# Kernel optimization log

Measured on AMD Instinct MI355X. Metric: run time of the kernel, lower is better.

Reference implementation:

```python
import jax, jax.numpy as jnp
import numpy as np

HIDDEN_DIM = 2048
NUM_HEADS = 16
HEAD_DIM = HIDDEN_DIM // NUM_HEADS
BATCH = 2
SEQ = 2048


def setup_inputs() -> dict:
    key = jax.random.key(0)
    ks = jax.random.split(key, 5)
    scale = 1.0 / np.sqrt(HIDDEN_DIM)
    x = jax.random.normal(ks[0], (BATCH, SEQ, HIDDEN_DIM), dtype=jnp.float32)
    w_q = jax.random.normal(ks[1], (HIDDEN_DIM, HIDDEN_DIM), dtype=jnp.float32) * scale
    w_k = jax.random.normal(ks[2], (HIDDEN_DIM, HIDDEN_DIM), dtype=jnp.float32) * scale
    w_v = jax.random.normal(ks[3], (HIDDEN_DIM, HIDDEN_DIM), dtype=jnp.float32) * scale
    w_o = jax.random.normal(ks[4], (HIDDEN_DIM, HIDDEN_DIM), dtype=jnp.float32) * scale
    return {"x": x, "w_q": w_q, "w_k": w_k, "w_v": w_v, "w_o": w_o}


def reference(x, w_q, w_k, w_v, w_o):
    # Projections: x @ W.T  (weights stored as (out, in) like torch)
    q = jnp.einsum('bsd,ed->bse', x, w_q)
    k = jnp.einsum('bsd,ed->bse', x, w_k)
    v = jnp.einsum('bsd,ed->bse', x, w_v)
    b, s, _ = q.shape
    # split heads: (b, h, s, hd)
    q = q.reshape(b, s, NUM_HEADS, HEAD_DIM).transpose(0, 2, 1, 3)
    k = k.reshape(b, s, NUM_HEADS, HEAD_DIM).transpose(0, 2, 1, 3)
    v = v.reshape(b, s, NUM_HEADS, HEAD_DIM).transpose(0, 2, 1, 3)
    scale = 1.0 / np.sqrt(HEAD_DIM)
    # Online-softmax tiling in the source (causal=False default) is
    # mathematically identical to standard softmax attention.
    scores = jnp.einsum('bhqd,bhkd->bhqk', q, k) * scale
    p = jax.nn.softmax(scores, axis=-1)
    o = jnp.einsum('bhqk,bhkd->bhqd', p, v)
    o = o.transpose(0, 2, 1, 3).reshape(b, s, HIDDEN_DIM)
    return jnp.einsum('bsd,ed->bse', o, w_o)
```

## Files before the change

kernel.cpp:

```cpp
#include <hip/hip_runtime.h>


typedef _Float16 half8 __attribute__((ext_vector_type(8)));
typedef _Float16 half4 __attribute__((ext_vector_type(4)));
typedef float floatx4 __attribute__((ext_vector_type(4)));

__device__ __forceinline__ void async16(const void* g, void* l) {
  __builtin_amdgcn_global_load_lds((__attribute__((address_space(1))) void*)(g),
                                   (__attribute__((address_space(3))) void*)(l),
                                   16, 0, 0);
}

__global__ void cvt_all(const float* __restrict__ x, const float* __restrict__ w0,
                        const float* __restrict__ w1, const float* __restrict__ w2,
                        const float* __restrict__ w3, _Float16* __restrict__ xh,
                        _Float16* __restrict__ wh, float scale0) {
  int i = blockIdx.x * blockDim.x + threadIdx.x;
  const int XQ = 1 << 21;
  float sc = 1.0f;
  const float* src;
  _Float16* dst;
  int j;
  if (i < XQ) { src = x; dst = xh; j = i; }
  else {
    int t = i - XQ;
    int m = t >> 20;
    src = (m == 0) ? w0 : (m == 1) ? w1 : (m == 2) ? w2 : w3;
    if (m == 0) sc = scale0;
    dst = wh; j = t;
  }
  int js = (i < XQ) ? j : (j & ((1 << 20) - 1));
  float4 v = reinterpret_cast<const float4*>(src)[js];
  union { _Float16 h[4]; short4 s; } u;
  u.h[0] = (_Float16)(v.x * sc); u.h[1] = (_Float16)(v.y * sc);
  u.h[2] = (_Float16)(v.z * sc); u.h[3] = (_Float16)(v.w * sc);
  reinterpret_cast<short4*>(dst)[j] = u.s;
}

template <int MO, int NO>
__device__ __forceinline__ void mmg(floatx4 (&acc)[4][4], const half8 (&af)[2][2],
                                    const half8 (&bf)[2][2]) {
#pragma unroll
  for (int mt = 0; mt < 2; ++mt)
#pragma unroll
    for (int nt = 0; nt < 2; ++nt)
#pragma unroll
      for (int ks = 0; ks < 2; ++ks)
        acc[MO + mt][NO + nt] = __builtin_amdgcn_mfma_f32_16x16x32_f16(
            af[mt][ks], bf[nt][ks], acc[MO + mt][NO + nt], 0, 0, 0);
}

__device__ __forceinline__ void rdfrag(half8 (&f)[2][2], const _Float16* base,
                                       int r0, int r1, int ch0, int ch1) {
  f[0][0] = *reinterpret_cast<const half8*>(base + r0 * 64 + ch0);
  f[0][1] = *reinterpret_cast<const half8*>(base + r0 * 64 + ch1);
  f[1][0] = *reinterpret_cast<const half8*>(base + r1 * 64 + ch0);
  f[1][1] = *reinterpret_cast<const half8*>(base + r1 * 64 + ch1);
}

template <int OUT_MODE>
__global__ __launch_bounds__(512, 2)
void gemm_nt(const _Float16* __restrict__ A, const _Float16* __restrict__ Bw,
             void* __restrict__ Cv, void* __restrict__ Cv2) {
  __shared__ _Float16 As[2][256 * 64];
  __shared__ _Float16 Bs[2][128 * 64];
  const int tid = threadIdx.x;
  const int wave = tid >> 6, lane = tid & 63;
  const int wm = wave >> 1, wn = wave & 1;
  const int l15 = lane & 15, l4 = lane >> 4;

  const int nwg = gridDim.x << 4;
  const int orig = blockIdx.x * 16 + blockIdx.y;
  const int swz = (orig & 7) * (nwg >> 3) + (orig >> 3);
  const int bm = swz & 15, bn = swz >> 4;

  const _Float16* ag[4]; int al[4];
#pragma unroll
  for (int j = 0; j < 4; ++j) {
    int c = j * 512 + tid, row = c >> 3, g = (c & 7) ^ (row & 7);
    ag[j] = A + (size_t)(bm * 256 + row) * 2048 + g * 8;
    al[j] = c * 8;
  }
  const _Float16* bg[2]; int bl[2];
#pragma unroll
  for (int j = 0; j < 2; ++j) {
    int c = j * 512 + tid, row = c >> 3, g = (c & 7) ^ (row & 7);
    bg[j] = Bw + (size_t)(bn * 128 + row) * 2048 + g * 8;
    bl[j] = c * 8;
  }

  const int rm = wm * 16 + l15;
  const int rn = wn * 16 + l15;
  const int ch0 = (l4 ^ (l15 & 7)) * 8;
  const int ch1 = ((l4 + 4) ^ (l15 & 7)) * 8;

#pragma unroll
  for (int j = 0; j < 4; ++j) async16(ag[j], &As[0][al[j]]);
#pragma unroll
  for (int j = 0; j < 2; ++j) async16(bg[j], &Bs[0][bl[j]]);
  asm volatile("s_waitcnt vmcnt(0)" ::: "memory");
  __builtin_amdgcn_s_barrier();

  floatx4 acc[4][4] = {};
  half8 afA[2][2], afB[2][2], bfA[2][2], bfB[2][2];

#pragma unroll 2
  for (int t = 0; t < 32; ++t) {
    const _Float16* Ac = &As[t & 1][0];
    const _Float16* Bc = &Bs[t & 1][0];
    _Float16* An = &As[(t & 1) ^ 1][0];
    _Float16* Bn = &Bs[(t & 1) ^ 1][0];
    const int kn = t * 64 + 64;
    const bool st = (t < 31);

    asm volatile("s_waitcnt vmcnt(3)" ::: "memory");
    rdfrag(afA, Ac, rm, rm + 64, ch0, ch1);
    if (st) { async16(ag[0] + kn, An + al[0]); async16(ag[1] + kn, An + al[1]); }
    __builtin_amdgcn_s_barrier();
    __builtin_amdgcn_s_waitcnt(0xC07F);
    __builtin_amdgcn_s_setprio(1);
    if (t) mmg<2, 2>(acc, afB, bfB);
    __builtin_amdgcn_s_setprio(0);
    __builtin_amdgcn_s_barrier();

    asm volatile("s_waitcnt vmcnt(4)" ::: "memory");
    rdfrag(bfA, Bc, rn, rn + 32, ch0, ch1);
    if (st) async16(bg[0] + kn, Bn + bl[0]);
    __builtin_amdgcn_s_barrier();
    __builtin_amdgcn_s_waitcnt(0xC07F);
    __builtin_amdgcn_s_setprio(1);
    mmg<0, 0>(acc, afA, bfA);
    __builtin_amdgcn_s_setprio(0);
    __builtin_amdgcn_s_barrier();

    asm volatile("s_waitcnt vmcnt(3)" ::: "memory");
    rdfrag(bfB, Bc, rn + 64, rn + 96, ch0, ch1);
    if (st) async16(bg[1] + kn, Bn + bl[1]);
    __builtin_amdgcn_s_barrier();
    __builtin_amdgcn_s_waitcnt(0xC07F);
    __builtin_amdgcn_s_setprio(1);
    mmg<0, 2>(acc, afA, bfB);
    __builtin_amdgcn_s_setprio(0);
    __builtin_amdgcn_s_barrier();

    asm volatile("s_waitcnt vmcnt(2)" ::: "memory");
    rdfrag(afB, Ac, rm + 128, rm + 192, ch0, ch1);
    if (st) { async16(ag[2] + kn, An + al[2]); async16(ag[3] + kn, An + al[3]); }
    __builtin_amdgcn_s_barrier();
    __builtin_amdgcn_s_waitcnt(0xC07F);
    __builtin_amdgcn_s_setprio(1);
    mmg<2, 0>(acc, afB, bfA);
    __builtin_amdgcn_s_setprio(0);
    __builtin_amdgcn_s_barrier();
  }
  mmg<2, 2>(acc, afB, bfB);

  const int cb = bn * 128;
  if constexpr (OUT_MODE == 0) {
    if (cb < 4096) {
      _Float16* C = (_Float16*)Cv + (size_t)(cb >> 11) * (4096ull * 2048);
#pragma unroll
      for (int mt = 0; mt < 4; ++mt)
#pragma unroll
        for (int nt = 0; nt < 4; ++nt) {
          int r0 = bm * 256 + mt * 64 + wm * 16 + l4 * 4;
          int cg = (cb + nt * 32 + wn * 16 + l15) & 2047;
#pragma unroll
          for (int r = 0; r < 4; ++r)
            C[(size_t)(r0 + r) * 2048 + cg] = (_Float16)acc[mt][nt][r];
        }
    } else {
      _Float16* C = (_Float16*)Cv2;
#pragma unroll
      for (int mt = 0; mt < 4; ++mt)
#pragma unroll
        for (int nt = 0; nt < 4; ++nt) {
          int m0 = bm * 256 + mt * 64 + wm * 16 + l4 * 4;
          int d = cb + nt * 32 + wn * 16 + l15 - 4096;
          size_t base = (size_t)(m0 >> 11) * (2048ull * 2048) + (size_t)d * 2048 + (m0 & 2047);
          union { _Float16 h[4]; short4 s; } u;
#pragma unroll
          for (int r = 0; r < 4; ++r) u.h[r] = (_Float16)acc[mt][nt][r];
          *reinterpret_cast<short4*>(C + base) = u.s;
        }
    }
  } else {
    float* C = (float*)Cv;
#pragma unroll
    for (int mt = 0; mt < 4; ++mt)
#pragma unroll
      for (int nt = 0; nt < 4; ++nt) {
        int r0 = bm * 256 + mt * 64 + wm * 16 + l4 * 4;
        int cg = cb + nt * 32 + wn * 16 + l15;
#pragma unroll
        for (int r = 0; r < 4; ++r)
          C[(size_t)(r0 + r) * 2048 + cg] = acc[mt][nt][r];
      }
  }
}

__global__ __launch_bounds__(256, 2)
void flash_attn(const _Float16* __restrict__ Q, const _Float16* __restrict__ Kg,
                const _Float16* __restrict__ Vt, _Float16* __restrict__ O) {
  __shared__ _Float16 Ks[64 * 128];
  __shared__ _Float16 Vs[128 * 64];
  __shared__ _Float16 Ps[128 * 64];
  const int tid = threadIdx.x, wave = tid >> 6, lane = tid & 63;
  const int l15 = lane & 15, l4 = lane >> 4;
  const int bh = blockIdx.y, b = bh >> 4, h = bh & 15;
  const int q0 = blockIdx.x * 128;

  const _Float16* Qp = Q + ((size_t)(b * 2048 + q0 + wave * 32)) * 2048 + h * 128;
  const _Float16* Kp = Kg + (size_t)b * 2048 * 2048 + h * 128;
  const _Float16* Vp = Vt + (size_t)b * 2048 * 2048 + (size_t)(h * 128) * 2048;

  half8 qf[2][4];
#pragma unroll
  for (int qt = 0; qt < 2; ++qt)
#pragma unroll
    for (int ks = 0; ks < 4; ++ks)
      qf[qt][ks] = *reinterpret_cast<const half8*>(
          Qp + (size_t)(qt * 16 + l15) * 2048 + ks * 32 + l4 * 8);

  floatx4 oacc[2][8] = {};
  float lsumq[2] = {0.f, 0.f};

  for (int k0 = 0; k0 < 2048; k0 += 64) {
    __syncthreads();
#pragma unroll
    for (int i = 0; i < 4; ++i) {
      int c = i * 256 + tid;
      int row = c >> 4, cc = c & 15;
      int g = cc ^ (row & 15);
      async16(Kp + (size_t)(k0 + row) * 2048 + g * 8, &Ks[c * 8]);
    }
#pragma unroll
    for (int i = 0; i < 4; ++i) {
      int c = i * 256 + tid;
      int row = c >> 3, cc = c & 7;
      int g = cc ^ (row & 7);
      async16(Vp + (size_t)row * 2048 + k0 + g * 8, &Vs[c * 8]);
    }
    __syncthreads();

    floatx4 sacc[4][2] = {};
#pragma unroll
    for (int ks = 0; ks < 4; ++ks) {
      half8 kf[4];
#pragma unroll
      for (int st = 0; st < 4; ++st) {
        int row = st * 16 + l15;
        int ch = (ks * 4 + l4) ^ l15;
        kf[st] = *reinterpret_cast<const half8*>(&Ks[row * 128 + ch * 8]);
      }
#pragma unroll
      for (int st = 0; st < 4; ++st)
#pragma unroll
        for (int qt = 0; qt < 2; ++qt)
          sacc[st][qt] = __builtin_amdgcn_mfma_f32_16x16x32_f16(kf[st], qf[qt][ks], sacc[st][qt], 0, 0, 0);
    }

#pragma unroll
    for (int qt = 0; qt < 2; ++qt)
#pragma unroll
      for (int st = 0; st < 4; ++st) {
        float p0 = exp2f(sacc[st][qt][0]);
        float p1 = exp2f(sacc[st][qt][1]);
        float p2 = exp2f(sacc[st][qt][2]);
        float p3 = exp2f(sacc[st][qt][3]);
        lsumq[qt] += (p0 + p1) + (p2 + p3);
        half4 pv;
        pv[0] = (_Float16)p0; pv[1] = (_Float16)p1;
        pv[2] = (_Float16)p2; pv[3] = (_Float16)p3;
        int ch = (st * 2 + (l4 >> 1)) ^ (l15 & 7);
        *reinterpret_cast<half4*>(
            &Ps[(wave * 32 + qt * 16 + l15) * 64 + ch * 8 + (l4 & 1) * 4]) = pv;
      }

    __builtin_amdgcn_s_waitcnt(0xC07F);

#pragma unroll
    for (int ks2 = 0; ks2 < 2; ++ks2) {
      half8 pf[2];
#pragma unroll
      for (int mt = 0; mt < 2; ++mt)
        pf[mt] = *reinterpret_cast<const half8*>(
            &Ps[(wave * 32 + mt * 16 + l15) * 64 + (((ks2 * 4 + l4) ^ (l15 & 7)) * 8)]);
#pragma unroll
      for (int nt2 = 0; nt2 < 8; ++nt2) {
        int row = nt2 * 16 + l15;
        int ch = (ks2 * 4 + l4) ^ (row & 7);
        half8 vf = *reinterpret_cast<const half8*>(&Vs[row * 64 + ch * 8]);
#pragma unroll
        for (int mt = 0; mt < 2; ++mt)
          oacc[mt][nt2] = __builtin_amdgcn_mfma_f32_16x16x32_f16(pf[mt], vf, oacc[mt][nt2], 0, 0, 0);
      }
    }
  }

#pragma unroll
  for (int qt = 0; qt < 2; ++qt) {
    lsumq[qt] += __shfl_xor(lsumq[qt], 16);
    lsumq[qt] += __shfl_xor(lsumq[qt], 32);
  }

  _Float16* Op = O + ((size_t)(b * 2048 + q0 + wave * 32)) * 2048 + h * 128;
#pragma unroll
  for (int mt = 0; mt < 2; ++mt)
#pragma unroll
    for (int r = 0; r < 4; ++r) {
      float inv = 1.0f / __shfl(lsumq[mt], l4 * 4 + r);
#pragma unroll
      for (int nt2 = 0; nt2 < 8; ++nt2) {
        int row = mt * 16 + l4 * 4 + r;
        int col = nt2 * 16 + l15;
        Op[(size_t)row * 2048 + col] = (_Float16)(oacc[mt][nt2][r] * inv);
      }
    }
}

extern "C" void kernel_launch(void* const* d_in, const int* in_sizes, int n_in,
                              void* d_out, int out_size, void* d_ws, size_t ws_size,
                              hipStream_t stream) {
  const float* x = (const float*)d_in[0];
  const float* wq = (const float*)d_in[1];
  const float* wk = (const float*)d_in[2];
  const float* wv = (const float*)d_in[3];
  const float* wo = (const float*)d_in[4];
  float* out = (float*)d_out;

  const size_t XN = (size_t)4096 * 2048;
  const size_t WN = (size_t)2048 * 2048;
  _Float16* xh = (_Float16*)d_ws;
  _Float16* qh = xh + XN;
  _Float16* vth = xh + 3 * XN;
  _Float16* oh = xh + 4 * XN;
  _Float16* wqh = xh + 5 * XN;

  const float SM_SCALE = 0.08838834764831845f * 1.4426950408889634f;

  cvt_all<<<dim3(24576), 256, 0, stream>>>(x, wq, wk, wv, wo, xh, wqh, SM_SCALE);
  gemm_nt<0><<<dim3(48, 16), 512, 0, stream>>>(xh, wqh, qh, vth);
  flash_attn<<<dim3(16, 32), 256, 0, stream>>>(qh, qh + XN, vth, oh);
  gemm_nt<2><<<dim3(16, 16), 512, 0, stream>>>(oh, wqh + 3 * WN, out, nullptr);
}
```

Measured before the change: 409.1 us.

## Enlarge projection GEMM tile to 256x256 with a 2x4 wave layout

The NT GEMM block tile grows from 256x128 to 256x256. Eight waves are arranged 2x4 and each wave holds an 8x4 set of 16x16 accumulators. The K loop is restructured into four phases with explicit vmcnt waits and a peeled final iteration, and the grid becomes 1D with a compile-time N-block count. The aim is to raise arithmetic intensity and cut global and LDS traffic per FLOP. In exchange, LDS use doubles to about 128KB per block, register pressure rises under the (512,2) launch bounds with a risk of spills, and the output projection launches only 128 blocks on a 256-CU device.

```diff
diff --git a/kernel.cpp b/kernel.cpp
--- a/kernel.cpp
+++ b/kernel.cpp
@@ -37,134 +37,156 @@
   reinterpret_cast<short4*>(dst)[j] = u.s;
 }
 
+__device__ __forceinline__ void rdA4(half8 (&f)[4][2], const _Float16* base,
+                                     int ch0, int ch1) {
+#pragma unroll
+  for (int mt = 0; mt < 4; ++mt) {
+    f[mt][0] = *reinterpret_cast<const half8*>(base + mt * 2048 + ch0);
+    f[mt][1] = *reinterpret_cast<const half8*>(base + mt * 2048 + ch1);
+  }
+}
+__device__ __forceinline__ void rdB2(half8 (&f)[2][2], const _Float16* base,
+                                     int ch0, int ch1) {
+#pragma unroll
+  for (int nt = 0; nt < 2; ++nt) {
+    f[nt][0] = *reinterpret_cast<const half8*>(base + nt * 4096 + ch0);
+    f[nt][1] = *reinterpret_cast<const half8*>(base + nt * 4096 + ch1);
+  }
+}
 template <int MO, int NO>
-__device__ __forceinline__ void mmg(floatx4 (&acc)[4][4], const half8 (&af)[2][2],
-                                    const half8 (&bf)[2][2]) {
-#pragma unroll
-  for (int mt = 0; mt < 2; ++mt)
-#pragma unroll
-    for (int nt = 0; nt < 2; ++nt)
-#pragma unroll
-      for (int ks = 0; ks < 2; ++ks)
+__device__ __forceinline__ void mmg16(floatx4 (&acc)[8][4], const half8 (&af)[4][2],
+                                      const half8 (&bf)[2][2]) {
+#pragma unroll
+  for (int kk = 0; kk < 2; ++kk)
+#pragma unroll
+    for (int mt = 0; mt < 4; ++mt)
+#pragma unroll
+      for (int nt = 0; nt < 2; ++nt)
         acc[MO + mt][NO + nt] = __builtin_amdgcn_mfma_f32_16x16x32_f16(
-            af[mt][ks], bf[nt][ks], acc[MO + mt][NO + nt], 0, 0, 0);
-}
-
-__device__ __forceinline__ void rdfrag(half8 (&f)[2][2], const _Float16* base,
-                                       int r0, int r1, int ch0, int ch1) {
-  f[0][0] = *reinterpret_cast<const half8*>(base + r0 * 64 + ch0);
-  f[0][1] = *reinterpret_cast<const half8*>(base + r0 * 64 + ch1);
-  f[1][0] = *reinterpret_cast<const half8*>(base + r1 * 64 + ch0);
-  f[1][1] = *reinterpret_cast<const half8*>(base + r1 * 64 + ch1);
-}
-
-template <int OUT_MODE>
+            af[mt][kk], bf[nt][kk], acc[MO + mt][NO + nt], 0, 0, 0);
+}
+
+template <int OUT_MODE, int NBN>
 __global__ __launch_bounds__(512, 2)
 void gemm_nt(const _Float16* __restrict__ A, const _Float16* __restrict__ Bw,
              void* __restrict__ Cv, void* __restrict__ Cv2) {
   __shared__ _Float16 As[2][256 * 64];
-  __shared__ _Float16 Bs[2][128 * 64];
+  __shared__ _Float16 Bs[2][256 * 64];
   const int tid = threadIdx.x;
   const int wave = tid >> 6, lane = tid & 63;
-  const int wm = wave >> 1, wn = wave & 1;
+  const int wm = wave >> 2, wn = wave & 3;
   const int l15 = lane & 15, l4 = lane >> 4;
 
-  const int nwg = gridDim.x << 4;
-  const int orig = blockIdx.x * 16 + blockIdx.y;
+  const int nwg = NBN * 16;
+  const int orig = blockIdx.x;
   const int swz = (orig & 7) * (nwg >> 3) + (orig >> 3);
-  const int bm = swz & 15, bn = swz >> 4;
-
-  const _Float16* ag[4]; int al[4];
-#pragma unroll
-  for (int j = 0; j < 4; ++j) {
-    int c = j * 512 + tid, row = c >> 3, g = (c & 7) ^ (row & 7);
-    ag[j] = A + (size_t)(bm * 256 + row) * 2048 + g * 8;
-    al[j] = c * 8;
-  }
-  const _Float16* bg[2]; int bl[2];
-#pragma unroll
-  for (int j = 0; j < 2; ++j) {
-    int c = j * 512 + tid, row = c >> 3, g = (c & 7) ^ (row & 7);
-    bg[j] = Bw + (size_t)(bn * 128 + row) * 2048 + g * 8;
-    bl[j] = c * 8;
-  }
-
-  const int rm = wm * 16 + l15;
-  const int rn = wn * 16 + l15;
+  const int bn = swz % NBN, bm = swz / NBN;
+
+  const int srow = tid >> 3;
+  const int g = (tid & 7) ^ (srow & 7);
+  const _Float16* ags = A + (size_t)(bm * 256 + srow) * 2048 + g * 8;
+  const _Float16* bgs = Bw + (size_t)(bn * 256 + srow) * 2048 + g * 8;
+  const int ldst = tid * 8;
+
+  const int arow = wm * 16 + l15;
+  const int brow = wn * 16 + l15;
   const int ch0 = (l4 ^ (l15 & 7)) * 8;
   const int ch1 = ((l4 + 4) ^ (l15 & 7)) * 8;
 
 #pragma unroll
-  for (int j = 0; j < 4; ++j) async16(ag[j], &As[0][al[j]]);
-#pragma unroll
-  for (int j = 0; j < 2; ++j) async16(bg[j], &Bs[0][bl[j]]);
+  for (int j = 0; j < 4; ++j) {
+    async16(ags + (size_t)j * 131072, &As[0][j * 4096 + ldst]);
+    async16(bgs + (size_t)j * 131072, &Bs[0][j * 4096 + ldst]);
+  }
   asm volatile("s_waitcnt vmcnt(0)" ::: "memory");
   __builtin_amdgcn_s_barrier();
 
-  floatx4 acc[4][4] = {};
-  half8 afA[2][2], afB[2][2], bfA[2][2], bfB[2][2];
-
-#pragma unroll 2
-  for (int t = 0; t < 32; ++t) {
-    const _Float16* Ac = &As[t & 1][0];
-    const _Float16* Bc = &Bs[t & 1][0];
-    _Float16* An = &As[(t & 1) ^ 1][0];
-    _Float16* Bn = &Bs[(t & 1) ^ 1][0];
+  floatx4 acc[8][4] = {};
+  half8 afA[4][2], afB[4][2], bfA[2][2], bfB[2][2];
+
+  for (int t = 0; t < 31; ++t) {
+    const int cur = t & 1, nxt = cur ^ 1;
     const int kn = t * 64 + 64;
-    const bool st = (t < 31);
-
-    asm volatile("s_waitcnt vmcnt(3)" ::: "memory");
-    rdfrag(afA, Ac, rm, rm + 64, ch0, ch1);
-    if (st) { async16(ag[0] + kn, An + al[0]); async16(ag[1] + kn, An + al[1]); }
+    const _Float16* Ab = &As[cur][arow * 64];
+    const _Float16* Bb = &Bs[cur][brow * 64];
+    _Float16* Asn = &As[nxt][ldst];
+    _Float16* Bsn = &Bs[nxt][ldst];
+
+    rdA4(afA, Ab, ch0, ch1);
+    async16(ags + kn, Asn);
+    async16(ags + 131072 + kn, Asn + 4096);
     __builtin_amdgcn_s_barrier();
     __builtin_amdgcn_s_waitcnt(0xC07F);
     __builtin_amdgcn_s_setprio(1);
-    if (t) mmg<2, 2>(acc, afB, bfB);
+    if (t) mmg16<4, 2>(acc, afB, bfB);
     __builtin_amdgcn_s_setprio(0);
-    __builtin_amdgcn_s_barrier();
-
+    asm volatile("s_waitcnt vmcnt(6)" ::: "memory");
+    __builtin_amdgcn_s_barrier();
+
+    rdB2(bfA, Bb, ch0, ch1);
+    async16(bgs + kn, Bsn);
+    async16(bgs + 131072 + kn, Bsn + 4096);
+    __builtin_amdgcn_s_barrier();
+    __builtin_amdgcn_s_waitcnt(0xC07F);
+    __builtin_amdgcn_s_setprio(1);
+    mmg16<0, 0>(acc, afA, bfA);
+    __builtin_amdgcn_s_setprio(0);
+    asm volatile("s_waitcnt vmcnt(6)" ::: "memory");
+    __builtin_amdgcn_s_barrier();
+
+    rdB2(bfB, Bb + 8192, ch0, ch1);
+    async16(bgs + 262144 + kn, Bsn + 8192);
+    async16(bgs + 393216 + kn, Bsn + 12288);
+    __builtin_amdgcn_s_barrier();
+    __builtin_amdgcn_s_waitcnt(0xC07F);
+    __builtin_amdgcn_s_setprio(1);
+    mmg16<0, 2>(acc, afA, bfB);
+    __builtin_amdgcn_s_setprio(0);
+    asm volatile("s_waitcnt vmcnt(6)" ::: "memory");
+    __builtin_amdgcn_s_barrier();
+
+    rdA4(afB, Ab + 8192, ch0, ch1);
+    async16(ags + 262144 + kn, Asn + 8192);
+    async16(ags + 393216 + kn, Asn + 12288);
+    __builtin_amdgcn_s_barrier();
+    __builtin_amdgcn_s_waitcnt(0xC07F);
+    __builtin_amdgcn_s_setprio(1);
+    mmg16<4, 0>(acc, afB, bfA);
+    __builtin_amdgcn_s_setprio(0);
+    asm volatile("s_waitcnt vmcnt(6)" ::: "memory");
+    __builtin_amdgcn_s_barrier();
+  }
+
+  {
+    const _Float16* Ab = &As[1][arow * 64];
+    const _Float16* Bb = &Bs[1][brow * 64];
+    rdA4(afA, Ab, ch0, ch1);
+    mmg16<4, 2>(acc, afB, bfB);
     asm volatile("s_waitcnt vmcnt(4)" ::: "memory");
-    rdfrag(bfA, Bc, rn, rn + 32, ch0, ch1);
-    if (st) async16(bg[0] + kn, Bn + bl[0]);
-    __builtin_amdgcn_s_barrier();
-    __builtin_amdgcn_s_waitcnt(0xC07F);
-    __builtin_amdgcn_s_setprio(1);
-    mmg<0, 0>(acc, afA, bfA);
-    __builtin_amdgcn_s_setprio(0);
-    __builtin_amdgcn_s_barrier();
-
-    asm volatile("s_waitcnt vmcnt(3)" ::: "memory");
-    rdfrag(bfB, Bc, rn + 64, rn + 96, ch0, ch1);
-    if (st) async16(bg[1] + kn, Bn + bl[1]);
-    __builtin_amdgcn_s_barrier();
-    __builtin_amdgcn_s_waitcnt(0xC07F);
-    __builtin_amdgcn_s_setprio(1);
-    mmg<0, 2>(acc, afA, bfB);
-    __builtin_amdgcn_s_setprio(0);
-    __builtin_amdgcn_s_barrier();
-
+    __builtin_amdgcn_s_barrier();
+    rdB2(bfA, Bb, ch0, ch1);
+    mmg16<0, 0>(acc, afA, bfA);
     asm volatile("s_waitcnt vmcnt(2)" ::: "memory");
-    rdfrag(afB, Ac, rm + 128, rm + 192, ch0, ch1);
-    if (st) { async16(ag[2] + kn, An + al[2]); async16(ag[3] + kn, An + al[3]); }
-    __builtin_amdgcn_s_barrier();
-    __builtin_amdgcn_s_waitcnt(0xC07F);
-    __builtin_amdgcn_s_setprio(1);
-    mmg<2, 0>(acc, afB, bfA);
-    __builtin_amdgcn_s_setprio(0);
-    __builtin_amdgcn_s_barrier();
-  }
-  mmg<2, 2>(acc, afB, bfB);
-
-  const int cb = bn * 128;
+    __builtin_amdgcn_s_barrier();
+    rdB2(bfB, Bb + 8192, ch0, ch1);
+    mmg16<0, 2>(acc, afA, bfB);
+    asm volatile("s_waitcnt vmcnt(0)" ::: "memory");
+    __builtin_amdgcn_s_barrier();
+    rdA4(afB, Ab + 8192, ch0, ch1);
+    mmg16<4, 0>(acc, afB, bfA);
+    mmg16<4, 2>(acc, afB, bfB);
+  }
+
+  const int cb0 = bn * 256;
   if constexpr (OUT_MODE == 0) {
-    if (cb < 4096) {
-      _Float16* C = (_Float16*)Cv + (size_t)(cb >> 11) * (4096ull * 2048);
-#pragma unroll
-      for (int mt = 0; mt < 4; ++mt)
+    if (cb0 < 4096) {
+      _Float16* C = (_Float16*)Cv + (size_t)(cb0 >> 11) * (4096ull * 2048);
+#pragma unroll
+      for (int mt = 0; mt < 8; ++mt)
 #pragma unroll
         for (int nt = 0; nt < 4; ++nt) {
-          int r0 = bm * 256 + mt * 64 + wm * 16 + l4 * 4;
-          int cg = (cb + nt * 32 + wn * 16 + l15) & 2047;
+          int r0 = bm * 256 + mt * 32 + wm * 16 + l4 * 4;
+          int cg = (cb0 + nt * 64 + wn * 16 + l15) & 2047;
 #pragma unroll
           for (int r = 0; r < 4; ++r)
             C[(size_t)(r0 + r) * 2048 + cg] = (_Float16)acc[mt][nt][r];
@@ -172,11 +194,11 @@
     } else {
       _Float16* C = (_Float16*)Cv2;
 #pragma unroll
-      for (int mt = 0; mt < 4; ++mt)
+      for (int mt = 0; mt < 8; ++mt)
 #pragma unroll
         for (int nt = 0; nt < 4; ++nt) {
-          int m0 = bm * 256 + mt * 64 + wm * 16 + l4 * 4;
-          int d = cb + nt * 32 + wn * 16 + l15 - 4096;
+          int m0 = bm * 256 + mt * 32 + wm * 16 + l4 * 4;
+          int d = cb0 + nt * 64 + wn * 16 + l15 - 4096;
           size_t base = (size_t)(m0 >> 11) * (2048ull * 2048) + (size_t)d * 2048 + (m0 & 2047);
           union { _Float16 h[4]; short4 s; } u;
 #pragma unroll
@@ -187,11 +209,11 @@
   } else {
     float* C = (float*)Cv;
 #pragma unroll
-    for (int mt = 0; mt < 4; ++mt)
+    for (int mt = 0; mt < 8; ++mt)
 #pragma unroll
       for (int nt = 0; nt < 4; ++nt) {
-        int r0 = bm * 256 + mt * 64 + wm * 16 + l4 * 4;
-        int cg = cb + nt * 32 + wn * 16 + l15;
+        int r0 = bm * 256 + mt * 32 + wm * 16 + l4 * 4;
+        int cg = cb0 + nt * 64 + wn * 16 + l15;
 #pragma unroll
         for (int r = 0; r < 4; ++r)
           C[(size_t)(r0 + r) * 2048 + cg] = acc[mt][nt][r];
@@ -340,7 +362,7 @@
   const float SM_SCALE = 0.08838834764831845f * 1.4426950408889634f;
 
   cvt_all<<<dim3(24576), 256, 0, stream>>>(x, wq, wk, wv, wo, xh, wqh, SM_SCALE);
-  gemm_nt<0><<<dim3(48, 16), 512, 0, stream>>>(xh, wqh, qh, vth);
+  gemm_nt<0, 24><<<dim3(384), 512, 0, stream>>>(xh, wqh, qh, vth);
   flash_attn<<<dim3(16, 32), 256, 0, stream>>>(qh, qh + XN, vth, oh);
-  gemm_nt<2><<<dim3(16, 16), 512, 0, stream>>>(oh, wqh + 3 * WN, out, nullptr);
-}
+  gemm_nt<2, 8><<<dim3(128), 512, 0, stream>>>(oh, wqh + 3 * WN, out, nullptr);
+}
```

New measurement: 403.2 us. About the same (-1.4%).
